# Performance work log

Hardware: AMD Instinct MI355X
Metric: run time of the kernel (lower is better)

Reference implementation:

```python
import jax, jax.numpy as jnp
import numpy as np

N_REL = 8


def setup_inputs() -> dict:
    key = jax.random.key(0)
    ks = jax.random.split(key, 16)
    N, E = 100_000, 1_600_000
    rn = lambda k, shape, s=0.1: jax.random.normal(k, shape, dtype=jnp.float32) * s
    return {
        "x": rn(ks[0], (N, 3), 1.0),
        "edge_index": jax.random.randint(ks[1], (2, E), 0, N),
        "edge_attr": rn(ks[2], (E, 2), 1.0),
        "edge_type": jax.random.randint(ks[3], (E,), 0, N_REL),
        "omega": rn(ks[4], (N, 2), 1.0),
        # encoder weights
        "Wn": rn(ks[5], (3, 64)), "bn": jnp.zeros((64,), jnp.float32),
        "We": rn(ks[6], (2, 32)), "be": jnp.zeros((32,), jnp.float32),
        "Wo": rn(ks[7], (2, 64)), "bo": jnp.zeros((64,), jnp.float32),
        # RGCN layer 1 (edge-feature-aware): per-relation W over concat(x_src, e) -> 64
        "W1": rn(ks[8], (N_REL, 96, 64)), "Wroot1": rn(ks[9], (64, 64)), "b1": jnp.zeros((64,), jnp.float32),
        # RGCN layer 2 (PyG RGCNConv, aggr='max')
        "W2": rn(ks[10], (N_REL, 64, 64)), "Wroot2": rn(ks[11], (64, 64)), "b2": jnp.zeros((64,), jnp.float32),
        # head
        "Wagg": rn(ks[12], (128, 64)), "bagg": jnp.zeros((64,), jnp.float32),
        "Wc": rn(ks[13], (64, 1)), "bc": jnp.zeros((1,), jnp.float32),
    }


def reference(x, edge_index, edge_attr, edge_type, omega,
              Wn, bn, We, be, Wo, bo,
              W1, Wroot1, b1, W2, Wroot2, b2,
              Wagg, bagg, Wc, bc):
    N = x.shape[0]
    n = jax.nn.relu(x @ Wn + bn)            # [N,64]
    e = jax.nn.relu(edge_attr @ We + be)    # [E,32]
    o = jax.nn.relu(omega @ Wo + bo)        # [N,64]
    src, dst = edge_index[0], edge_index[1]

    # --- RGCN layer 1: per-relation transform of [x_src || e], sum-aggregate ---
    feat = jnp.concatenate([n[src], e], axis=1)  # [E,96]
    acc = n @ Wroot1 + b1                        # root/self term
    for r in range(N_REL):
        m = (edge_type == r).astype(feat.dtype)[:, None]
        acc = acc + jax.ops.segment_sum((feat * m) @ W1[r], dst, num_segments=N)
    h = jax.nn.relu(acc)                         # [N,64]

    # --- RGCN layer 2: per-relation transform of x_src, max-aggregate per relation, sum over relations ---
    hs = h[src]                                  # [E,64]
    neg = jnp.finfo(h.dtype).min
    acc2 = h @ Wroot2 + b2
    for r in range(N_REL):
        mask = (edge_type == r)[:, None]
        msg = jnp.where(mask, hs @ W2[r], neg)
        mx = jax.ops.segment_max(msg, dst, num_segments=N)
        acc2 = acc2 + jnp.where(mx > neg * 0.5, mx, 0.0)  # empty segments -> 0 (PyG zeros-init scatter)
    h2 = jax.nn.relu(acc2)                       # [N,64]

    out = jax.nn.relu(jnp.concatenate([h2, o], axis=1) @ Wagg + bagg)
    return jnp.tanh(out @ Wc + bc) * 5.0
```

## Files before the change

kernel.cpp:

```cpp
#include <hip/hip_runtime.h>
#include <cmath>

typedef __attribute__((ext_vector_type(8))) short short8;
typedef __attribute__((ext_vector_type(4))) float floatx4;

__device__ __forceinline__ unsigned short rnbf(float f) {
    unsigned u = __float_as_uint(f);
    u += 0x7fffu + ((u >> 16) & 1u);
    return (unsigned short)(u >> 16);
}
__device__ __forceinline__ float bf2f(unsigned short h) {
    return __uint_as_float(((unsigned)h) << 16);
}
__device__ __forceinline__ int rfl(int v) { return __builtin_amdgcn_readfirstlane(v); }
__device__ __forceinline__ float eAct(unsigned ry, float we0, float we1, float bev) {
    float a0 = __uint_as_float(ry & 0xFFFF0000u);
    float a1 = __uint_as_float(ry << 16);
    return fmaxf(fmaf(a1, we1, fmaf(a0, we0, bev)), 0.f);
}
__device__ __forceinline__ unsigned vidx(int x, unsigned pl, int lane) {
    return (((unsigned)x >> 24) & 7u)*pl + (unsigned)(x & 0xFFFFFF)*64u + (unsigned)lane;
}
__device__ __forceinline__ void mstep(int r, float v, int& cur, float& mx, float& add) {
    bool nb = (r != cur);
    add += nb ? mx : 0.f;
    mx = nb ? v : fmaxf(mx, v);
    cur = r;
}

__global__ void k_histd(const int* __restrict__ ei, const int* __restrict__ et,
                        int* __restrict__ deg8, int E)
{
    int e = blockIdx.x*blockDim.x + threadIdx.x;
    if (e < E) atomicAdd(&deg8[ei[E + e]*8 + et[e]], 1);
}

#define SCHUNK 1024
__global__ void k_bsum(const int* __restrict__ deg, int* __restrict__ bsum, int K)
{
    __shared__ int s[256];
    int b = blockIdx.x, t = threadIdx.x;
    int base = b*SCHUNK;
    int v = 0;
    for (int k = t; k < SCHUNK; k += 256) { int i = base + k; v += (i < K) ? deg[i] : 0; }
    s[t] = v; __syncthreads();
    for (int o = 128; o; o >>= 1) { if (t < o) s[t] += s[t+o]; __syncthreads(); }
    if (t == 0) bsum[b] = s[0];
}
__global__ void k_bscan(int* __restrict__ bsum, int nb)
{
    __shared__ int ts[256];
    int t = threadIdx.x;
    int v[4]; int loc = 0;
    #pragma unroll
    for (int u = 0; u < 4; ++u) { int i = t*4+u; v[u] = (i < nb) ? bsum[i] : 0; loc += v[u]; }
    ts[t] = loc; __syncthreads();
    for (int o = 1; o < 256; o <<= 1) {
        int add = (t >= o) ? ts[t-o] : 0;
        __syncthreads();
        ts[t] += add;
        __syncthreads();
    }
    int excl = ts[t] - loc;
    #pragma unroll
    for (int u = 0; u < 4; ++u) {
        int i = t*4+u;
        if (i < nb) bsum[i] = excl;
        excl += v[u];
    }
}
__global__ void k_bapply(const int* __restrict__ deg, const int* __restrict__ bsum,
                         int* __restrict__ off, int* __restrict__ cursor, int K)
{
    __shared__ int ts[256];
    int b = blockIdx.x, t = threadIdx.x;
    int base = b*SCHUNK;
    int v[4]; int loc = 0;
    #pragma unroll
    for (int u = 0; u < 4; ++u) { int i = base + t*4 + u; v[u] = (i < K) ? deg[i] : 0; loc += v[u]; }
    ts[t] = loc; __syncthreads();
    for (int o = 1; o < 256; o <<= 1) {
        int add = (t >= o) ? ts[t-o] : 0;
        __syncthreads();
        ts[t] += add;
        __syncthreads();
    }
    int excl = ts[t] - loc + bsum[b];
    #pragma unroll
    for (int u = 0; u < 4; ++u) {
        int i = base + t*4 + u;
        if (i < K) { off[i] = excl; cursor[i] = excl; }
        excl += v[u];
        if (i == K-1) off[K] = excl;
    }
}

__global__ void k_scatd(const int* __restrict__ ei, const float* __restrict__ ea,
                        const int* __restrict__ et, int* __restrict__ cursor,
                        int2* __restrict__ srec, int E)
{
    int e = blockIdx.x*blockDim.x + threadIdx.x;
    if (e >= E) return;
    int rel = et[e];
    int key = ei[E + e]*8 + rel;
    int pos = atomicAdd(&cursor[key], 1);
    float2 a = ((const float2*)ea)[e];
    int xv = ei[e] | (rel << 24);
    int yv = ((int)rnbf(a.x) << 16) | (int)rnbf(a.y);
    srec[pos] = make_int2(xv, yv);
}

#define PB_KEYS 4096
#define PA_CH   4096
__global__ void k_binit(const int* __restrict__ off8, int* __restrict__ bktCur,
                        int nbkt, int K8)
{
    int b = blockIdx.x*blockDim.x + threadIdx.x;
    if (b < nbkt) {
        int k = b*PB_KEYS; if (k > K8) k = K8;
        bktCur[b] = off8[k];
    }
}
__global__ __launch_bounds__(256) void k_partA(
    const int* __restrict__ ei, const float* __restrict__ ea,
    const int* __restrict__ et, int* __restrict__ bktCur,
    int2* __restrict__ tmp, int E, int nbkt)
{
    __shared__ int cnt[512], base[512];
    int b0 = blockIdx.x * PA_CH;
    for (int j = threadIdx.x; j < nbkt; j += 256) cnt[j] = 0;
    __syncthreads();
    int2 rec[16]; int bk[16];
    #pragma unroll
    for (int u = 0; u < 16; ++u) {
        int e = b0 + u*256 + threadIdx.x;
        bk[u] = -1;
        if (e < E) {
            int rel = et[e];
            int src = ei[e];
            int dst = ei[E + e];
            float2 a = ((const float2*)ea)[e];
            rec[u] = make_int2(src | (rel << 17) | ((dst & 511) << 20),
                               ((int)rnbf(a.x) << 16) | (int)rnbf(a.y));
            bk[u] = dst >> 9;
            atomicAdd(&cnt[bk[u]], 1);
        }
    }
    __syncthreads();
    for (int j = threadIdx.x; j < nbkt; j += 256) {
        int c = cnt[j];
        base[j] = c ? atomicAdd(&bktCur[j], c) : 0;
    }
    __syncthreads();
    for (int j = threadIdx.x; j < nbkt; j += 256) cnt[j] = 0;
    __syncthreads();
    #pragma unroll
    for (int u = 0; u < 16; ++u) {
        if (bk[u] >= 0) {
            int pos = base[bk[u]] + atomicAdd(&cnt[bk[u]], 1);
            tmp[pos] = rec[u];
        }
    }
}
__global__ __launch_bounds__(256) void k_partB(
    const int2* __restrict__ tmp, const int* __restrict__ off8,
    int2* __restrict__ srec, int K8)
{
    __shared__ int cur[PB_KEYS];
    int kbase = blockIdx.x * PB_KEYS;
    int kend = kbase + PB_KEYS; if (kend > K8) kend = K8;
    int nk = kend - kbase;
    for (int j = threadIdx.x; j < nk; j += 256) cur[j] = off8[kbase + j];
    __syncthreads();
    int bstart = off8[kbase];
    int bend = off8[kend];
    for (int i = bstart + threadIdx.x; i < bend; i += 256) {
        int2 r = tmp[i];
        unsigned xw = (unsigned)r.x;
        int src = (int)(xw & 0x1FFFFu);
        int rel = (int)((xw >> 17) & 7u);
        int dstLow = (int)((xw >> 20) & 511u);
        int pos = atomicAdd(&cur[dstLow*8 + rel], 1);
        srec[pos] = make_int2(src | (rel << 24), r.y);
    }
}

__global__ __launch_bounds__(64) void k_wpack(
    const float* __restrict__ W1, const float* __restrict__ W2,
    const float* __restrict__ Wroot1, const float* __restrict__ Wroot2,
    const float* __restrict__ Wagg, unsigned short* __restrict__ wpk)
{
    int unit = blockIdx.x >> 2;
    int jt = blockIdx.x & 3;
    int lane = threadIdx.x;
    const float* Wb;
    int kbase;
    if (unit < 16) {
        Wb = W1 + (size_t)(unit >> 1)*96*64;
        kbase = (unit & 1)*32;
    } else if (unit < 32) {
        Wb = W2 + (size_t)((unit - 16) >> 1)*64*64;
        kbase = ((unit - 16) & 1)*32;
    } else if (unit < 40) {
        Wb = W1 + (size_t)(unit - 32)*96*64;
        kbase = 64;
    } else if (unit < 42) {
        Wb = Wroot1; kbase = (unit - 40)*32;
    } else if (unit < 44) {
        Wb = Wroot2; kbase = (unit - 42)*32;
    } else {
        Wb = Wagg;   kbase = (unit - 44)*32;
    }
    int j = jt*16 + (lane & 15);
    size_t base = (((size_t)unit*4 + jt)*64 + lane)*16;
    #pragma unroll
    for (int i = 0; i < 8; ++i) {
        int k = kbase + (lane >> 4)*8 + i;
        float f = Wb[(size_t)k*64 + j];
        unsigned short hi = rnbf(f);
        unsigned short lo = rnbf(f - bf2f(hi));
        wpk[base + i] = hi;
        wpk[base + 8 + i] = lo;
    }
}

__global__ __launch_bounds__(256) void k_encB(
    const float* __restrict__ x,
    const float* __restrict__ Wn, const float* __restrict__ bn,
    const unsigned short* __restrict__ wpk, const float* __restrict__ b1,
    float* __restrict__ nbuf, float* __restrict__ acc1, int N)
{
    int lane = threadIdx.x & 63;
    int wave = threadIdx.x >> 6;
    int n0 = blockIdx.x*64 + 16*wave;
    int m = lane & 15, q = lane >> 4;
    #pragma unroll 4
    for (int t = 0; t < 16; ++t) {
        int nd = n0 + t;
        if (nd < N) {
            float x0 = x[3*nd], x1 = x[3*nd+1], x2 = x[3*nd+2];
            float nj = fmaxf(fmaf(x2, Wn[128+lane], fmaf(x1, Wn[64+lane], fmaf(x0, Wn[lane], bn[lane]))), 0.f);
            nbuf[(size_t)nd*64 + lane] = nj;
        }
    }
    int node = n0 + m; if (node >= N) node = N - 1;
    float x0 = x[3*node], x1 = x[3*node+1], x2 = x[3*node+2];
    short8 ah[2], al[2];
    #pragma unroll
    for (int ks = 0; ks < 2; ++ks) {
        #pragma unroll
        for (int i = 0; i < 8; ++i) {
            int f = ks*32 + q*8 + i;
            float nf = fmaxf(fmaf(x2, Wn[128+f], fmaf(x1, Wn[64+f], fmaf(x0, Wn[f], bn[f]))), 0.f);
            unsigned short hb = rnbf(nf);
            ah[ks][i] = (short)hb;
            al[ks][i] = (short)rnbf(nf - bf2f(hb));
        }
    }
    floatx4 acc[4];
    #pragma unroll
    for (int jt = 0; jt < 4; ++jt) acc[jt] = (floatx4){0.f,0.f,0.f,0.f};
    #pragma unroll
    for (int ks = 0; ks < 2; ++ks) {
        int unit = 40 + ks;
        #pragma unroll
        for (int jt = 0; jt < 4; ++jt) {
            const unsigned short* qp = wpk + (((size_t)unit*4 + jt)*64 + lane)*16;
            short8 bh = *(const short8*)qp;
            short8 bl = *(const short8*)(qp + 8);
            acc[jt] = __builtin_amdgcn_mfma_f32_16x16x32_bf16(ah[ks], bh, acc[jt], 0,0,0);
            acc[jt] = __builtin_amdgcn_mfma_f32_16x16x32_bf16(ah[ks], bl, acc[jt], 0,0,0);
            acc[jt] = __builtin_amdgcn_mfma_f32_16x16x32_bf16(al[ks], bh, acc[jt], 0,0,0);
        }
    }
    #pragma unroll
    for (int jt = 0; jt < 4; ++jt) {
        float bb = b1[jt*16 + m];
        #pragma unroll
        for (int t = 0; t < 4; ++t) {
            int row = n0 + q*4 + t;
            if (row < N) acc1[(size_t)row*64 + jt*16 + m] = acc[jt][t] + bb;
        }
    }
}

__global__ __launch_bounds__(256) void k_vgemmB(
    const float* __restrict__ F, const unsigned short* __restrict__ wpk,
    int unitBase, int g0, int Gc, unsigned short* __restrict__ Vbf,
    size_t plane, int N)
{
    int lane = threadIdx.x & 63;
    int wave = threadIdx.x >> 6;
    int n0 = blockIdx.x*64 + 16*wave;
    int m = lane & 15, q = lane >> 4;
    int node = n0 + m;
    if (node >= N) node = N - 1;
    const float4* Fr = (const float4*)(F + (size_t)node*64);
    short8 ah[2], al[2];
    #pragma unroll
    for (int ks = 0; ks < 2; ++ks) {
        float4 u0 = Fr[ks*8 + q*2];
        float4 u1 = Fr[ks*8 + q*2 + 1];
        float fv[8] = {u0.x,u0.y,u0.z,u0.w,u1.x,u1.y,u1.z,u1.w};
        #pragma unroll
        for (int i = 0; i < 8; ++i) {
            unsigned short hb = rnbf(fv[i]);
            ah[ks][i] = (short)hb;
            al[ks][i] = (short)rnbf(fv[i] - bf2f(hb));
        }
    }
    for (int p = 0; p < Gc; ++p) {
        int rel = g0 + p;
        floatx4 acc[4];
        #pragma unroll
        for (int jt = 0; jt < 4; ++jt) acc[jt] = (floatx4){0.f,0.f,0.f,0.f};
        #pragma unroll
        for (int ks = 0; ks < 2; ++ks) {
            int unit = unitBase + rel*2 + ks;
            #pragma unroll
            for (int jt = 0; jt < 4; ++jt) {
                const unsigned short* qp = wpk + (((size_t)unit*4 + jt)*64 + lane)*16;
                short8 bh = *(const short8*)qp;
                short8 bl = *(const short8*)(qp + 8);
                acc[jt] = __builtin_amdgcn_mfma_f32_16x16x32_bf16(ah[ks], bh, acc[jt], 0,0,0);
                acc[jt] = __builtin_amdgcn_mfma_f32_16x16x32_bf16(ah[ks], bl, acc[jt], 0,0,0);
                acc[jt] = __builtin_amdgcn_mfma_f32_16x16x32_bf16(al[ks], bh, acc[jt], 0,0,0);
            }
        }
        unsigned short* Vp = Vbf + (size_t)p*plane;
        #pragma unroll
        for (int jt = 0; jt < 4; ++jt) {
            #pragma unroll
            for (int t = 0; t < 4; ++t) {
                int row = n0 + q*4 + t;
                if (row < N) Vp[(size_t)row*64 + jt*16 + m] = rnbf(acc[jt][t]);
            }
        }
    }
}

__global__ __launch_bounds__(256) void k_agg1ef(
    const int2* __restrict__ srec, const int* __restrict__ off8,
    const unsigned short* __restrict__ Vbf, size_t plane,
    const float* __restrict__ We, const float* __restrict__ be,
    float* __restrict__ acc1, unsigned short* __restrict__ Sep, int N)
{
    int lane = threadIdx.x & 63;
    int wv = threadIdx.x >> 6;
    unsigned pl = (unsigned)plane;
    float we0 = We[lane & 31], we1 = We[32 + (lane & 31)], bev = be[lane & 31];
    int stride = gridDim.x*4;
    for (int node = blockIdx.x*4 + wv; node < N; node += stride) {
        const int* ofp = off8 + node*8;
        int o0 = rfl(ofp[0]), o8 = rfl(ofp[8]);
        float vsum = 0.f;
        int i = o0;
        for (; i + 16 <= o8; i += 16) {
            int2 q[16];
            #pragma unroll
            for (int u = 0; u < 16; ++u) q[u] = srec[i+u];
            int xs[16];
            #pragma unroll
            for (int u = 0; u < 16; ++u) xs[u] = rfl(q[u].x);
            float v[16];
            #pragma unroll
            for (int u = 0; u < 16; ++u) v[u] = bf2f(Vbf[vidx(xs[u], pl, lane)]);
            float s01 = (v[0]+v[1]) + (v[2]+v[3]);
            float s23 = (v[4]+v[5]) + (v[6]+v[7]);
            float s45 = (v[8]+v[9]) + (v[10]+v[11]);
            float s67 = (v[12]+v[13]) + (v[14]+v[15]);
            vsum += (s01 + s23) + (s45 + s67);
        }
        for (; i + 8 <= o8; i += 8) {
            int2 q0 = srec[i+0], q1 = srec[i+1], q2 = srec[i+2], q3 = srec[i+3];
            int2 q4 = srec[i+4], q5 = srec[i+5], q6 = srec[i+6], q7 = srec[i+7];
            int x0 = rfl(q0.x), x1 = rfl(q1.x), x2 = rfl(q2.x), x3 = rfl(q3.x);
            int x4 = rfl(q4.x), x5 = rfl(q5.x), x6 = rfl(q6.x), x7 = rfl(q7.x);
            float v0 = bf2f(Vbf[vidx(x0, pl, lane)]);
            float v1 = bf2f(Vbf[vidx(x1, pl, lane)]);
            float v2 = bf2f(Vbf[vidx(x2, pl, lane)]);
            float v3 = bf2f(Vbf[vidx(x3, pl, lane)]);
            float v4 = bf2f(Vbf[vidx(x4, pl, lane)]);
            float v5 = bf2f(Vbf[vidx(x5, pl, lane)]);
            float v6 = bf2f(Vbf[vidx(x6, pl, lane)]);
            float v7 = bf2f(Vbf[vidx(x7, pl, lane)]);
            vsum += ((v0+v1)+(v2+v3)) + ((v4+v5)+(v6+v7));
        }
        for (; i < o8; ++i) {
            int xx = rfl(srec[i].x);
            vsum += bf2f(Vbf[vidx(xx, pl, lane)]);
        }
        int o1 = rfl(ofp[1]), o2 = rfl(ofp[2]), o3 = rfl(ofp[3]), o4 = rfl(ofp[4]);
        int o5 = rfl(ofp[5]), o6 = rfl(ofp[6]), o7 = rfl(ofp[7]);
        const unsigned* sy = (const unsigned*)srec;
        float se0=0,se1=0,se2=0,se3=0,se4=0,se5=0,se6=0,se7=0;
        #pragma unroll
        for (int r = 0; r < 8; ++r) {
            int s = (r==0)?o0:(r==1)?o1:(r==2)?o2:(r==3)?o3:(r==4)?o4:(r==5)?o5:(r==6)?o6:o7;
            int e = (r==0)?o1:(r==1)?o2:(r==2)?o3:(r==3)?o4:(r==4)?o5:(r==5)?o6:(r==6)?o7:o8;
            if (s == e) continue;
            float ev = 0.f;
            int k = s;
            for (; k + 4 <= e; k += 4) {
                unsigned y0 = sy[2*(k+0)+1], y1 = sy[2*(k+1)+1];
                unsigned y2 = sy[2*(k+2)+1], y3 = sy[2*(k+3)+1];
                ev += eAct(y0, we0, we1, bev);
                ev += eAct(y1, we0, we1, bev);
                ev += eAct(y2, we0, we1, bev);
                ev += eAct(y3, we0, we1, bev);
            }
            for (; k < e; ++k) ev += eAct(sy[2*k+1], we0, we1, bev);
            if (r == 0) se0 = ev;  if (r == 1) se1 = ev;
            if (r == 2) se2 = ev;  if (r == 3) se3 = ev;
            if (r == 4) se4 = ev;  if (r == 5) se5 = ev;
            if (r == 6) se6 = ev;  if (r == 7) se7 = ev;
        }
        unsigned short* Sp = Sep + (size_t)node*256;
        Sp[0*64 + lane] = rnbf((lane < 32) ? se0 : se1);
        Sp[1*64 + lane] = rnbf((lane < 32) ? se2 : se3);
        Sp[2*64 + lane] = rnbf((lane < 32) ? se4 : se5);
        Sp[3*64 + lane] = rnbf((lane < 32) ? se6 : se7);
        if (o0 != o8) acc1[(size_t)node*64 + lane] += vsum;
    }
}

__global__ __launch_bounds__(256) void k_agg1e(
    const int2* __restrict__ srec, const int* __restrict__ off8,
    const unsigned short* __restrict__ Vbf, size_t plane,
    const float* __restrict__ We, const float* __restrict__ be,
    float* __restrict__ acc1, unsigned short* __restrict__ Sep, int N, int Gc)
{
    int lane = threadIdx.x & 63;
    int wv = threadIdx.x >> 6;
    float we0 = We[lane & 31], we1 = We[32 + (lane & 31)], bev = be[lane & 31];
    int stride = gridDim.x*4;
    for (int node = blockIdx.x*4 + wv; node < N; node += stride) {
        int o0 = rfl(off8[node*8+0]), o1 = rfl(off8[node*8+1]), o2 = rfl(off8[node*8+2]);
        int o3 = rfl(off8[node*8+3]), o4 = rfl(off8[node*8+4]), o5 = rfl(off8[node*8+5]);
        int o6 = rfl(off8[node*8+6]), o7 = rfl(off8[node*8+7]), o8 = rfl(off8[node*8+8]);
        float vsum = 0.f;
        float se0=0,se1=0,se2=0,se3=0,se4=0,se5=0,se6=0,se7=0;
        #pragma unroll
        for (int r = 0; r < 8; ++r) {
            int s = (r==0)?o0:(r==1)?o1:(r==2)?o2:(r==3)?o3:(r==4)?o4:(r==5)?o5:(r==6)?o6:o7;
            int e = (r==0)?o1:(r==1)?o2:(r==2)?o3:(r==3)?o4:(r==4)?o5:(r==5)?o6:(r==6)?o7:o8;
            if (s == e) continue;
            const unsigned short* Vp = Vbf + (size_t)r*plane;
            bool doV = (r < Gc);
            float ev = 0.f;
            int i = s;
            for (; i + 8 <= e; i += 8) {
                int2 q0 = srec[i+0], q1 = srec[i+1], q2 = srec[i+2], q3 = srec[i+3];
                int2 q4 = srec[i+4], q5 = srec[i+5], q6 = srec[i+6], q7 = srec[i+7];
                if (doV) {
                    float v0 = bf2f(Vp[(size_t)(rfl(q0.x) & 0xFFFFFF)*64 + lane]);
                    float v1 = bf2f(Vp[(size_t)(rfl(q1.x) & 0xFFFFFF)*64 + lane]);
                    float v2 = bf2f(Vp[(size_t)(rfl(q2.x) & 0xFFFFFF)*64 + lane]);
                    float v3 = bf2f(Vp[(size_t)(rfl(q3.x) & 0xFFFFFF)*64 + lane]);
                    float v4 = bf2f(Vp[(size_t)(rfl(q4.x) & 0xFFFFFF)*64 + lane]);
                    float v5 = bf2f(Vp[(size_t)(rfl(q5.x) & 0xFFFFFF)*64 + lane]);
                    float v6 = bf2f(Vp[(size_t)(rfl(q6.x) & 0xFFFFFF)*64 + lane]);
                    float v7 = bf2f(Vp[(size_t)(rfl(q7.x) & 0xFFFFFF)*64 + lane]);
                    vsum += ((v0+v1)+(v2+v3)) + ((v4+v5)+(v6+v7));
                }
                ev += eAct((unsigned)q0.y, we0, we1, bev);
                ev += eAct((unsigned)q1.y, we0, we1, bev);
                ev += eAct((unsigned)q2.y, we0, we1, bev);
                ev += eAct((unsigned)q3.y, we0, we1, bev);
                ev += eAct((unsigned)q4.y, we0, we1, bev);
                ev += eAct((unsigned)q5.y, we0, we1, bev);
                ev += eAct((unsigned)q6.y, we0, we1, bev);
                ev += eAct((unsigned)q7.y, we0, we1, bev);
            }
            for (; i < e; ++i) {
                int2 qq = srec[i];
                if (doV) vsum += bf2f(Vp[(size_t)(rfl(qq.x) & 0xFFFFFF)*64 + lane]);
                ev += eAct((unsigned)qq.y, we0, we1, bev);
            }
            if (r == 0) se0 = ev;  if (r == 1) se1 = ev;
            if (r == 2) se2 = ev;  if (r == 3) se3 = ev;
            if (r == 4) se4 = ev;  if (r == 5) se5 = ev;
            if (r == 6) se6 = ev;  if (r == 7) se7 = ev;
        }
        unsigned short* Sp = Sep + (size_t)node*256;
        Sp[0*64 + lane] = rnbf((lane < 32) ? se0 : se1);
        Sp[1*64 + lane] = rnbf((lane < 32) ? se2 : se3);
        Sp[2*64 + lane] = rnbf((lane < 32) ? se4 : se5);
        Sp[3*64 + lane] = rnbf((lane < 32) ? se6 : se7);
        if (o0 != o8) acc1[(size_t)node*64 + lane] += vsum;
    }
}

__global__ __launch_bounds__(256) void k_agg1v(
    const int2* __restrict__ srec, const int* __restrict__ off8,
    const unsigned short* __restrict__ Vbf, size_t plane,
    float* __restrict__ acc1, int N, int g0, int g1)
{
    int lane = threadIdx.x & 63;
    int wv = threadIdx.x >> 6;
    int stride = gridDim.x*4;
    for (int node = blockIdx.x*4 + wv; node < N; node += stride) {
        float vsum = 0.f;
        bool any = false;
        for (int r = g0; r < g1; ++r) {
            int s = rfl(off8[node*8 + r]);
            int e = rfl(off8[node*8 + r + 1]);
            if (s == e) continue;
            any = true;
            const unsigned short* Vp = Vbf + (size_t)(r - g0)*plane;
            int i = s;
            for (; i + 8 <= e; i += 8) {
                int s0 = rfl(srec[i+0].x) & 0xFFFFFF, s1 = rfl(srec[i+1].x) & 0xFFFFFF;
                int s2 = rfl(srec[i+2].x) & 0xFFFFFF, s3 = rfl(srec[i+3].x) & 0xFFFFFF;
                int s4 = rfl(srec[i+4].x) & 0xFFFFFF, s5 = rfl(srec[i+5].x) & 0xFFFFFF;
                int s6 = rfl(srec[i+6].x) & 0xFFFFFF, s7 = rfl(srec[i+7].x) & 0xFFFFFF;
                float v0 = bf2f(Vp[(size_t)s0*64 + lane]), v1 = bf2f(Vp[(size_t)s1*64 + lane]);
                float v2 = bf2f(Vp[(size_t)s2*64 + lane]), v3 = bf2f(Vp[(size_t)s3*64 + lane]);
                float v4 = bf2f(Vp[(size_t)s4*64 + lane]), v5 = bf2f(Vp[(size_t)s5*64 + lane]);
                float v6 = bf2f(Vp[(size_t)s6*64 + lane]), v7 = bf2f(Vp[(size_t)s7*64 + lane]);
                vsum += ((v0+v1)+(v2+v3)) + ((v4+v5)+(v6+v7));
            }
            for (; i < e; ++i) {
                int sx = rfl(srec[i].x) & 0xFFFFFF;
                vsum += bf2f(Vp[(size_t)sx*64 + lane]);
            }
        }
        if (any) acc1[(size_t)node*64 + lane] += vsum;
    }
}

__global__ __launch_bounds__(256) void k_segemm(
    const unsigned short* __restrict__ Sep, const unsigned short* __restrict__ wpk,
    float* __restrict__ acc1, int N)
{
    int lane = threadIdx.x & 63;
    int wave = threadIdx.x >> 6;
    int n0 = blockIdx.x*64 + 16*wave;
    int m = lane & 15, q = lane >> 4;
    int node = n0 + m;
    if (node >= N) node = N - 1;
    floatx4 acc[4];
    #pragma unroll
    for (int jt = 0; jt < 4; ++jt) acc[jt] = (floatx4){0.f,0.f,0.f,0.f};
    for (int rel = 0; rel < 8; ++rel) {
        short8 ah = *(const short8*)(Sep + (size_t)node*256 + rel*32 + q*8);
        int unit = 32 + rel;
        #pragma unroll
        for (int jt = 0; jt < 4; ++jt) {
            const unsigned short* qp = wpk + (((size_t)unit*4 + jt)*64 + lane)*16;
            short8 bh = *(const short8*)qp;
            short8 bl = *(const short8*)(qp + 8);
            acc[jt] = __builtin_amdgcn_mfma_f32_16x16x32_bf16(ah, bh, acc[jt], 0,0,0);
            acc[jt] = __builtin_amdgcn_mfma_f32_16x16x32_bf16(ah, bl, acc[jt], 0,0,0);
        }
    }
    #pragma unroll
    for (int jt = 0; jt < 4; ++jt) {
        #pragma unroll
        for (int t = 0; t < 4; ++t) {
            int row = n0 + q*4 + t;
            if (row < N) acc1[(size_t)row*64 + jt*16 + m] += acc[jt][t];
        }
    }
}

__global__ __launch_bounds__(256) void k_hrowB(
    float* __restrict__ acc1, float* __restrict__ acc2,
    const unsigned short* __restrict__ wpk, const float* __restrict__ b2, int N)
{
    int lane = threadIdx.x & 63;
    int wave = threadIdx.x >> 6;
    int n0 = blockIdx.x*64 + 16*wave;
    int m = lane & 15, q = lane >> 4;
    int node = n0 + m;
    if (node >= N) node = N - 1;
    float4* Fr = (float4*)(acc1 + (size_t)node*64);
    short8 ah[2], al[2];
    #pragma unroll
    for (int ks = 0; ks < 2; ++ks) {
        float4 u0 = Fr[ks*8 + q*2];
        float4 u1 = Fr[ks*8 + q*2 + 1];
        float fv[8] = {u0.x,u0.y,u0.z,u0.w,u1.x,u1.y,u1.z,u1.w};
        #pragma unroll
        for (int i = 0; i < 8; ++i) {
            float hv = fmaxf(fv[i], 0.f);
            fv[i] = hv;
            unsigned short hb = rnbf(hv);
            ah[ks][i] = (short)hb;
            al[ks][i] = (short)rnbf(hv - bf2f(hb));
        }
        Fr[ks*8 + q*2]     = make_float4(fv[0], fv[1], fv[2], fv[3]);
        Fr[ks*8 + q*2 + 1] = make_float4(fv[4], fv[5], fv[6], fv[7]);
    }
    floatx4 acc[4];
    #pragma unroll
    for (int jt = 0; jt < 4; ++jt) acc[jt] = (floatx4){0.f,0.f,0.f,0.f};
    #pragma unroll
    for (int ks = 0; ks < 2; ++ks) {
        int unit = 42 + ks;
        #pragma unroll
        for (int jt = 0; jt < 4; ++jt) {
            const unsigned short* qp = wpk + (((size_t)unit*4 + jt)*64 + lane)*16;
            short8 bh = *(const short8*)qp;
            short8 bl = *(const short8*)(qp + 8);
            acc[jt] = __builtin_amdgcn_mfma_f32_16x16x32_bf16(ah[ks], bh, acc[jt], 0,0,0);
            acc[jt] = __builtin_amdgcn_mfma_f32_16x16x32_bf16(ah[ks], bl, acc[jt], 0,0,0);
            acc[jt] = __builtin_amdgcn_mfma_f32_16x16x32_bf16(al[ks], bh, acc[jt], 0,0,0);
        }
    }
    #pragma unroll
    for (int jt = 0; jt < 4; ++jt) {
        float bb = b2[jt*16 + m];
        #pragma unroll
        for (int t = 0; t < 4; ++t) {
            int row = n0 + q*4 + t;
            if (row < N) acc2[(size_t)row*64 + jt*16 + m] = acc[jt][t] + bb;
        }
    }
}

__global__ __launch_bounds__(256) void k_agg2f(
    const int2* __restrict__ srec, const int* __restrict__ off8,
    const unsigned short* __restrict__ Ubf, size_t plane,
    float* __restrict__ acc2, int N)
{
    int lane = threadIdx.x & 63;
    int wv = threadIdx.x >> 6;
    unsigned pl = (unsigned)plane;
    int stride = gridDim.x*4;
    for (int node = blockIdx.x*4 + wv; node < N; node += stride) {
        int o0 = rfl(off8[node*8]);
        int o8 = rfl(off8[node*8 + 8]);
        if (o0 == o8) continue;
        float add = 0.f, mx = 0.f;
        int cur = -1;
        int i = o0;
        for (; i + 16 <= o8; i += 16) {
            int2 q[16];
            #pragma unroll
            for (int u = 0; u < 16; ++u) q[u] = srec[i+u];
            int xs[16];
            #pragma unroll
            for (int u = 0; u < 16; ++u) xs[u] = rfl(q[u].x);
            float v[16];
            #pragma unroll
            for (int u = 0; u < 16; ++u) v[u] = bf2f(Ubf[vidx(xs[u], pl, lane)]);
            #pragma unroll
            for (int u = 0; u < 16; ++u)
                mstep((int)(((unsigned)xs[u] >> 24) & 7u), v[u], cur, mx, add);
        }
        for (; i + 8 <= o8; i += 8) {
            int2 q0 = srec[i+0], q1 = srec[i+1], q2 = srec[i+2], q3 = srec[i+3];
            int2 q4 = srec[i+4], q5 = srec[i+5], q6 = srec[i+6], q7 = srec[i+7];
            int x0 = rfl(q0.x), x1 = rfl(q1.x), x2 = rfl(q2.x), x3 = rfl(q3.x);
            int x4 = rfl(q4.x), x5 = rfl(q5.x), x6 = rfl(q6.x), x7 = rfl(q7.x);
            float v0 = bf2f(Ubf[vidx(x0, pl, lane)]);
            float v1 = bf2f(Ubf[vidx(x1, pl, lane)]);
            float v2 = bf2f(Ubf[vidx(x2, pl, lane)]);
            float v3 = bf2f(Ubf[vidx(x3, pl, lane)]);
            float v4 = bf2f(Ubf[vidx(x4, pl, lane)]);
            float v5 = bf2f(Ubf[vidx(x5, pl, lane)]);
            float v6 = bf2f(Ubf[vidx(x6, pl, lane)]);
            float v7 = bf2f(Ubf[vidx(x7, pl, lane)]);
            mstep((int)(((unsigned)x0 >> 24) & 7u), v0, cur, mx, add);
            mstep((int)(((unsigned)x1 >> 24) & 7u), v1, cur, mx, add);
            mstep((int)(((unsigned)x2 >> 24) & 7u), v2, cur, mx, add);
            mstep((int)(((unsigned)x3 >> 24) & 7u), v3, cur, mx, add);
            mstep((int)(((unsigned)x4 >> 24) & 7u), v4, cur, mx, add);
            mstep((int)(((unsigned)x5 >> 24) & 7u), v5, cur, mx, add);
            mstep((int)(((unsigned)x6 >> 24) & 7u), v6, cur, mx, add);
            mstep((int)(((unsigned)x7 >> 24) & 7u), v7, cur, mx, add);
        }
        for (; i < o8; ++i) {
            int xx = rfl(srec[i].x);
            float v = bf2f(Ubf[vidx(xx, pl, lane)]);
            mstep((int)(((unsigned)xx >> 24) & 7u), v, cur, mx, add);
        }
        add += mx;
        acc2[(size_t)node*64 + lane] += add;
    }
}

__global__ __launch_bounds__(256) void k_agg2(
    const int2* __restrict__ srec, const int* __restrict__ off8,
    const unsigned short* __restrict__ Ubf, size_t plane,
    float* __restrict__ acc2, int N, int g0, int g1)
{
    int lane = threadIdx.x & 63;
    int wv = threadIdx.x >> 6;
    int stride = gridDim.x*4;
    const float NEG = -__builtin_inff();
    for (int node = blockIdx.x*4 + wv; node < N; node += stride) {
        float add = 0.f;
        bool any = false;
        for (int r = g0; r < g1; ++r) {
            int s = rfl(off8[node*8 + r]);
            int e = rfl(off8[node*8 + r + 1]);
            if (s == e) continue;
            any = true;
            const unsigned short* Up = Ubf + (size_t)(r - g0)*plane;
            float mx = NEG;
            int i = s;
            for (; i + 8 <= e; i += 8) {
                int s0 = rfl(srec[i+0].x) & 0xFFFFFF, s1 = rfl(srec[i+1].x) & 0xFFFFFF;
                int s2 = rfl(srec[i+2].x) & 0xFFFFFF, s3 = rfl(srec[i+3].x) & 0xFFFFFF;
                int s4 = rfl(srec[i+4].x) & 0xFFFFFF, s5 = rfl(srec[i+5].x) & 0xFFFFFF;
                int s6 = rfl(srec[i+6].x) & 0xFFFFFF, s7 = rfl(srec[i+7].x) & 0xFFFFFF;
                float v0 = bf2f(Up[(size_t)s0*64 + lane]), v1 = bf2f(Up[(size_t)s1*64 + lane]);
                float v2 = bf2f(Up[(size_t)s2*64 + lane]), v3 = bf2f(Up[(size_t)s3*64 + lane]);
                float v4 = bf2f(Up[(size_t)s4*64 + lane]), v5 = bf2f(Up[(size_t)s5*64 + lane]);
                float v6 = bf2f(Up[(size_t)s6*64 + lane]), v7 = bf2f(Up[(size_t)s7*64 + lane]);
                float m01 = fmaxf(v0, v1), m23 = fmaxf(v2, v3);
                float m45 = fmaxf(v4, v5), m67 = fmaxf(v6, v7);
                mx = fmaxf(mx, fmaxf(fmaxf(m01, m23), fmaxf(m45, m67)));
            }
            for (; i < e; ++i) {
                int sx = rfl(srec[i].x) & 0xFFFFFF;
                mx = fmaxf(mx, bf2f(Up[(size_t)sx*64 + lane]));
            }
            add += mx;
        }
        if (any) acc2[(size_t)node*64 + lane] += add;
    }
}

__global__ __launch_bounds__(256) void k_finB(
    const float* __restrict__ acc2, const float* __restrict__ omega,
    const float* __restrict__ Wo, const float* __restrict__ bo,
    const unsigned short* __restrict__ wpk,
    const float* __restrict__ bagg, const float* __restrict__ Wc,
    const float* __restrict__ bc, float* __restrict__ out, int N)
{
    int lane = threadIdx.x & 63;
    int wave = threadIdx.x >> 6;
    int n0 = blockIdx.x*64 + 16*wave;
    int m = lane & 15, q = lane >> 4;
    int node = n0 + m;
    if (node >= N) node = N - 1;
    short8 ah[4], al[4];
    const float4* Fr = (const float4*)(acc2 + (size_t)node*64);
    #pragma unroll
    for (int ks = 0; ks < 2; ++ks) {
        float4 u0 = Fr[ks*8 + q*2];
        float4 u1 = Fr[ks*8 + q*2 + 1];
        float fv[8] = {u0.x,u0.y,u0.z,u0.w,u1.x,u1.y,u1.z,u1.w};
        #pragma unroll
        for (int i = 0; i < 8; ++i) {
            float hv = fmaxf(fv[i], 0.f);
            unsigned short hb = rnbf(hv);
            ah[ks][i] = (short)hb;
            al[ks][i] = (short)rnbf(hv - bf2f(hb));
        }
    }
    float om0 = omega[2*node], om1 = omega[2*node+1];
    #pragma unroll
    for (int ks = 2; ks < 4; ++ks) {
        #pragma unroll
        for (int i = 0; i < 8; ++i) {
            int f = (ks - 2)*32 + q*8 + i;
            float ov = fmaxf(fmaf(om1, Wo[64+f], fmaf(om0, Wo[f], bo[f])), 0.f);
            unsigned short hb = rnbf(ov);
            ah[ks][i] = (short)hb;
            al[ks][i] = (short)rnbf(ov - bf2f(hb));
        }
    }
    floatx4 acc[4];
    #pragma unroll
    for (int jt = 0; jt < 4; ++jt) acc[jt] = (floatx4){0.f,0.f,0.f,0.f};
    #pragma unroll
    for (int ks = 0; ks < 4; ++ks) {
        int unit = 44 + ks;
        #pragma unroll
        for (int jt = 0; jt < 4; ++jt) {
            const unsigned short* qp = wpk + (((size_t)unit*4 + jt)*64 + lane)*16;
            short8 bh = *(const short8*)qp;
            short8 bl = *(const short8*)(qp + 8);
            acc[jt] = __builtin_amdgcn_mfma_f32_16x16x32_bf16(ah[ks], bh, acc[jt], 0,0,0);
            acc[jt] = __builtin_amdgcn_mfma_f32_16x16x32_bf16(ah[ks], bl, acc[jt], 0,0,0);
            acc[jt] = __builtin_amdgcn_mfma_f32_16x16x32_bf16(al[ks], bh, acc[jt], 0,0,0);
        }
    }
    float bg0 = bagg[m], bg1 = bagg[16+m], bg2 = bagg[32+m], bg3 = bagg[48+m];
    float wc0 = Wc[m],   wc1 = Wc[16+m],   wc2 = Wc[32+m],   wc3 = Wc[48+m];
    float bc0 = bc[0];
    #pragma unroll
    for (int t = 0; t < 4; ++t) {
        float s = fmaxf(acc[0][t] + bg0, 0.f)*wc0
                + fmaxf(acc[1][t] + bg1, 0.f)*wc1
                + fmaxf(acc[2][t] + bg2, 0.f)*wc2
                + fmaxf(acc[3][t] + bg3, 0.f)*wc3;
        s += __shfl_xor(s, 1);
        s += __shfl_xor(s, 2);
        s += __shfl_xor(s, 4);
        s += __shfl_xor(s, 8);
        int row = n0 + q*4 + t;
        if (m == 0 && row < N) out[row] = tanhf(s + bc0) * 5.0f;
    }
}

extern "C" void kernel_launch(void* const* d_in, const int* in_sizes, int n_in,
                              void* d_out, int out_size, void* d_ws, size_t ws_size,
                              hipStream_t stream)
{
    const float* x      = (const float*)d_in[0];
    const int*   ei     = (const int*)d_in[1];
    const float* ea     = (const float*)d_in[2];
    const int*   et     = (const int*)d_in[3];
    const float* omega  = (const float*)d_in[4];
    const float* Wn     = (const float*)d_in[5];
    const float* bn     = (const float*)d_in[6];
    const float* We     = (const float*)d_in[7];
    const float* be     = (const float*)d_in[8];
    const float* Wo     = (const float*)d_in[9];
    const float* bo     = (const float*)d_in[10];
    const float* W1     = (const float*)d_in[11];
    const float* Wroot1 = (const float*)d_in[12];
    const float* b1     = (const float*)d_in[13];
    const float* W2     = (const float*)d_in[14];
    const float* Wroot2 = (const float*)d_in[15];
    const float* b2     = (const float*)d_in[16];
    const float* Wagg   = (const float*)d_in[17];
    const float* bagg   = (const float*)d_in[18];
    const float* Wc     = (const float*)d_in[19];
    const float* bc     = (const float*)d_in[20];
    int N = in_sizes[0] / 3;
    int E = in_sizes[3];
    float* out = (float*)d_out;

    int K8 = N*8;
    int nb = (K8 + SCHUNK - 1)/SCHUNK;

    #define ALIGN256(p) ((char*)(((size_t)(p) + 255) & ~(size_t)255))
    char* pp = (char*)d_ws;
    float* nbuf   = (float*)pp;  pp = ALIGN256(pp + (size_t)N*64*4);
    float* acc1   = (float*)pp;  pp = ALIGN256(pp + (size_t)N*64*4);
    int2*  srec   = (int2*)pp;   pp = ALIGN256(pp + (size_t)E*8);
    int*   deg8   = (int*)pp;    pp = ALIGN256(pp + (size_t)K8*4);
    int*   off8   = (int*)pp;    pp = ALIGN256(pp + (size_t)(K8+1)*4);
    int*   cursor = (int*)pp;    pp = ALIGN256(pp + (size_t)K8*4);
    int*   bsum   = (int*)pp;    pp = ALIGN256(pp + (size_t)nb*4);
    int*   bktCur = (int*)pp;    pp = ALIGN256(pp + (size_t)512*4);
    unsigned short* wpk = (unsigned short*)pp;
    pp = ALIGN256(pp + (size_t)48*4*64*16*2);
    unsigned short* Sepool = (unsigned short*)pp;
    pp = ALIGN256(pp + (size_t)N*256*2);
    size_t off = (size_t)(pp - (char*)d_ws);
    size_t planeElems = (size_t)N*64;
    size_t avail = (ws_size > off) ? (ws_size - off) : 0;
    int G = (int)(avail / (planeElems*2));
    if (G > 8) G = 8;
    if (G < 1) G = 1;
    unsigned short* Vbf = (unsigned short*)pp;
    float* acc2 = nbuf;

    int gblocks = (N + 63)/64;
    k_wpack<<<192, 64, 0, stream>>>(W1, W2, Wroot1, Wroot2, Wagg, wpk);
    k_encB<<<gblocks, 256, 0, stream>>>(x, Wn, bn, wpk, b1, nbuf, acc1, N);
    hipMemsetAsync(deg8, 0, (size_t)K8*4, stream);
    k_histd<<<(E + 255)/256, 256, 0, stream>>>(ei, et, deg8, E);
    k_bsum<<<nb, 256, 0, stream>>>(deg8, bsum, K8);
    k_bscan<<<1, 256, 0, stream>>>(bsum, nb);
    k_bapply<<<nb, 256, 0, stream>>>(deg8, bsum, off8, cursor, K8);

    int nbkt = (N + 511) >> 9;
    bool fastSort = (N <= 131072) && ((size_t)E*8 <= (size_t)N*256*2);
    if (fastSort) {
        int2* tmp = (int2*)Sepool;
        k_binit<<<(nbkt + 255)/256, 256, 0, stream>>>(off8, bktCur, nbkt, K8);
        k_partA<<<(E + PA_CH - 1)/PA_CH, 256, 0, stream>>>(ei, ea, et, bktCur, tmp, E, nbkt);
        k_partB<<<nbkt, 256, 0, stream>>>(tmp, off8, srec, K8);
    } else {
        k_scatd<<<(E + 255)/256, 256, 0, stream>>>(ei, ea, et, cursor, srec, E);
    }

    int aggBlocks = 4096;
    if (G == 8) {
        k_vgemmB<<<gblocks, 256, 0, stream>>>(nbuf, wpk, 0, 0, 8, Vbf, planeElems, N);
        k_agg1ef<<<aggBlocks, 256, 0, stream>>>(srec, off8, Vbf, planeElems, We, be,
                                                acc1, Sepool, N);
    } else {
        int Gc1 = G;
        k_vgemmB<<<gblocks, 256, 0, stream>>>(nbuf, wpk, 0, 0, Gc1, Vbf, planeElems, N);
        k_agg1e<<<aggBlocks, 256, 0, stream>>>(srec, off8, Vbf, planeElems, We, be,
                                               acc1, Sepool, N, Gc1);
        for (int g0 = Gc1; g0 < 8; g0 += G) {
            int Gc = (8 - g0 < G) ? (8 - g0) : G;
            k_vgemmB<<<gblocks, 256, 0, stream>>>(nbuf, wpk, 0, g0, Gc, Vbf, planeElems, N);
            k_agg1v<<<aggBlocks, 256, 0, stream>>>(srec, off8, Vbf, planeElems,
                                                   acc1, N, g0, g0 + Gc);
        }
    }
    k_segemm<<<gblocks, 256, 0, stream>>>(Sepool, wpk, acc1, N);
    k_hrowB<<<gblocks, 256, 0, stream>>>(acc1, acc2, wpk, b2, N);
    if (G == 8) {
        k_vgemmB<<<gblocks, 256, 0, stream>>>(acc1, wpk, 16, 0, 8, Vbf, planeElems, N);
        k_agg2f<<<aggBlocks, 256, 0, stream>>>(srec, off8, Vbf, planeElems, acc2, N);
    } else {
        for (int g0 = 0; g0 < 8; g0 += G) {
            int Gc = (8 - g0 < G) ? (8 - g0) : G;
            k_vgemmB<<<gblocks, 256, 0, stream>>>(acc1, wpk, 16, g0, Gc, Vbf, planeElems, N);
            k_agg2<<<aggBlocks, 256, 0, stream>>>(srec, off8, Vbf, planeElems,
                                                  acc2, N, g0, g0 + Gc);
        }
    }
    k_finB<<<gblocks, 256, 0, stream>>>(acc2, omega, Wo, bo, wpk, bagg, Wc, bc, out, N);
}
```

Before: 546.1 us.

## Fuse encoder/root/V-gemm kernels and replace full key histogram with bucket-level sort

Fuses the node encoder, layer-1 root GEMM and per-relation V projection into one kernel (k_encV), and fuses the edge-feature segment GEMM, ReLU, layer-2 root GEMM and layer-2 V projection into another (k_seghrowV). This removes the intermediate nbuf round-trip and several launches. The fast sort path drops the full per-(dst,rel) histogram and three-kernel scan. It uses a coarse 512-node bucket count instead, and each partB2 block computes its own fine offsets in shared memory. The cost is recomputing the encoder activations inside each fused kernel and extra shared-memory scan work per bucket.

```diff
diff --git a/kernel.cpp b/kernel.cpp
--- a/kernel.cpp
+++ b/kernel.cpp
@@ -34,7 +34,6 @@
     int e = blockIdx.x*blockDim.x + threadIdx.x;
     if (e < E) atomicAdd(&deg8[ei[E + e]*8 + et[e]], 1);
 }
-
 #define SCHUNK 1024
 __global__ void k_bsum(const int* __restrict__ deg, int* __restrict__ bsum, int K)
 {
@@ -94,7 +93,6 @@
         if (i == K-1) off[K] = excl;
     }
 }
-
 __global__ void k_scatd(const int* __restrict__ ei, const float* __restrict__ ea,
                         const int* __restrict__ et, int* __restrict__ cursor,
                         int2* __restrict__ srec, int E)
@@ -112,14 +110,37 @@
 
 #define PB_KEYS 4096
 #define PA_CH   4096
-__global__ void k_binit(const int* __restrict__ off8, int* __restrict__ bktCur,
-                        int nbkt, int K8)
-{
-    int b = blockIdx.x*blockDim.x + threadIdx.x;
-    if (b < nbkt) {
-        int k = b*PB_KEYS; if (k > K8) k = K8;
-        bktCur[b] = off8[k];
-    }
+__global__ __launch_bounds__(256) void k_cnt256(
+    const int* __restrict__ ei, int* __restrict__ bktCnt, int E, int nbkt)
+{
+    __shared__ int cnt[512];
+    for (int j = threadIdx.x; j < nbkt; j += 256) cnt[j] = 0;
+    __syncthreads();
+    int stride = gridDim.x*256;
+    for (int e = blockIdx.x*256 + threadIdx.x; e < E; e += stride)
+        atomicAdd(&cnt[ei[E + e] >> 9], 1);
+    __syncthreads();
+    for (int j = threadIdx.x; j < nbkt; j += 256) {
+        int c = cnt[j];
+        if (c) atomicAdd(&bktCnt[j], c);
+    }
+}
+__global__ void k_scan256(const int* __restrict__ bktCnt, int* __restrict__ bktBase,
+                          int* __restrict__ bktCur, int nbkt)
+{
+    __shared__ int ts[256];
+    int t = threadIdx.x;
+    int v = (t < nbkt) ? bktCnt[t] : 0;
+    ts[t] = v; __syncthreads();
+    for (int o = 1; o < 256; o <<= 1) {
+        int add = (t >= o) ? ts[t-o] : 0;
+        __syncthreads();
+        ts[t] += add;
+        __syncthreads();
+    }
+    int excl = ts[t] - v;
+    if (t < nbkt) { bktBase[t] = excl; bktCur[t] = excl; }
+    if (t == nbkt - 1) bktBase[nbkt] = excl + v;
 }
 __global__ __launch_bounds__(256) void k_partA(
     const int* __restrict__ ei, const float* __restrict__ ea,
@@ -162,25 +183,54 @@
         }
     }
 }
-__global__ __launch_bounds__(256) void k_partB(
-    const int2* __restrict__ tmp, const int* __restrict__ off8,
-    int2* __restrict__ srec, int K8)
-{
-    __shared__ int cur[PB_KEYS];
-    int kbase = blockIdx.x * PB_KEYS;
+__global__ __launch_bounds__(256) void k_partB2(
+    const int2* __restrict__ tmp, const int* __restrict__ bktBase,
+    int* __restrict__ off8, int2* __restrict__ srec, int K8)
+{
+    __shared__ int cnt[PB_KEYS];
+    __shared__ int ts[256];
+    int b = blockIdx.x;
+    int kbase = b * PB_KEYS;
     int kend = kbase + PB_KEYS; if (kend > K8) kend = K8;
     int nk = kend - kbase;
-    for (int j = threadIdx.x; j < nk; j += 256) cur[j] = off8[kbase + j];
+    int bstart = bktBase[b];
+    int bend = bktBase[b + 1];
+    int t = threadIdx.x;
+    for (int j = t; j < PB_KEYS; j += 256) cnt[j] = 0;
     __syncthreads();
-    int bstart = off8[kbase];
-    int bend = off8[kend];
-    for (int i = bstart + threadIdx.x; i < bend; i += 256) {
+    for (int i = bstart + t; i < bend; i += 256) {
+        unsigned xw = (unsigned)tmp[i].x;
+        int key = (int)((xw >> 20) & 511u)*8 + (int)((xw >> 17) & 7u);
+        atomicAdd(&cnt[key], 1);
+    }
+    __syncthreads();
+    int loc[16]; int lsum = 0;
+    #pragma unroll
+    for (int u = 0; u < 16; ++u) { loc[u] = cnt[t*16 + u]; lsum += loc[u]; }
+    ts[t] = lsum; __syncthreads();
+    for (int o = 1; o < 256; o <<= 1) {
+        int add = (t >= o) ? ts[t-o] : 0;
+        __syncthreads();
+        ts[t] += add;
+        __syncthreads();
+    }
+    int excl = ts[t] - lsum + bstart;
+    #pragma unroll
+    for (int u = 0; u < 16; ++u) {
+        int j = t*16 + u;
+        cnt[j] = excl;
+        if (j < nk) off8[kbase + j] = excl;
+        excl += loc[u];
+    }
+    if (t == 0 && kend == K8) off8[K8] = bend;
+    __syncthreads();
+    for (int i = bstart + t; i < bend; i += 256) {
         int2 r = tmp[i];
         unsigned xw = (unsigned)r.x;
         int src = (int)(xw & 0x1FFFFu);
         int rel = (int)((xw >> 17) & 7u);
-        int dstLow = (int)((xw >> 20) & 511u);
-        int pos = atomicAdd(&cur[dstLow*8 + rel], 1);
+        int key = (int)((xw >> 20) & 511u)*8 + rel;
+        int pos = atomicAdd(&cnt[key], 1);
         srec[pos] = make_int2(src | (rel << 24), r.y);
     }
 }
@@ -221,6 +271,87 @@
         unsigned short lo = rnbf(f - bf2f(hi));
         wpk[base + i] = hi;
         wpk[base + 8 + i] = lo;
+    }
+}
+
+__global__ __launch_bounds__(256) void k_encV(
+    const float* __restrict__ x,
+    const float* __restrict__ Wn, const float* __restrict__ bn,
+    const unsigned short* __restrict__ wpk, const float* __restrict__ b1,
+    float* __restrict__ acc1, unsigned short* __restrict__ Vbf,
+    size_t plane, int N)
+{
+    int lane = threadIdx.x & 63;
+    int wave = threadIdx.x >> 6;
+    int n0 = blockIdx.x*64 + 16*wave;
+    int m = lane & 15, q = lane >> 4;
+    int node = n0 + m; if (node >= N) node = N - 1;
+    float x0 = x[3*node], x1 = x[3*node+1], x2 = x[3*node+2];
+    short8 ah[2], al[2];
+    #pragma unroll
+    for (int ks = 0; ks < 2; ++ks) {
+        #pragma unroll
+        for (int i = 0; i < 8; ++i) {
+            int f = ks*32 + q*8 + i;
+            float nf = fmaxf(fmaf(x2, Wn[128+f], fmaf(x1, Wn[64+f], fmaf(x0, Wn[f], bn[f]))), 0.f);
+            unsigned short hb = rnbf(nf);
+            ah[ks][i] = (short)hb;
+            al[ks][i] = (short)rnbf(nf - bf2f(hb));
+        }
+    }
+    {
+        floatx4 acc[4];
+        #pragma unroll
+        for (int jt = 0; jt < 4; ++jt) acc[jt] = (floatx4){0.f,0.f,0.f,0.f};
+        #pragma unroll
+        for (int ks = 0; ks < 2; ++ks) {
+            int unit = 40 + ks;
+            #pragma unroll
+            for (int jt = 0; jt < 4; ++jt) {
+                const unsigned short* qp = wpk + (((size_t)unit*4 + jt)*64 + lane)*16;
+                short8 bh = *(const short8*)qp;
+                short8 bl = *(const short8*)(qp + 8);
+                acc[jt] = __builtin_amdgcn_mfma_f32_16x16x32_bf16(ah[ks], bh, acc[jt], 0,0,0);
+                acc[jt] = __builtin_amdgcn_mfma_f32_16x16x32_bf16(ah[ks], bl, acc[jt], 0,0,0);
+                acc[jt] = __builtin_amdgcn_mfma_f32_16x16x32_bf16(al[ks], bh, acc[jt], 0,0,0);
+            }
+        }
+        #pragma unroll
+        for (int jt = 0; jt < 4; ++jt) {
+            float bb = b1[jt*16 + m];
+            #pragma unroll
+            for (int t = 0; t < 4; ++t) {
+                int row = n0 + q*4 + t;
+                if (row < N) acc1[(size_t)row*64 + jt*16 + m] = acc[jt][t] + bb;
+            }
+        }
+    }
+    for (int p = 0; p < 8; ++p) {
+        floatx4 acc[4];
+        #pragma unroll
+        for (int jt = 0; jt < 4; ++jt) acc[jt] = (floatx4){0.f,0.f,0.f,0.f};
+        #pragma unroll
+        for (int ks = 0; ks < 2; ++ks) {
+            int unit = p*2 + ks;
+            #pragma unroll
+            for (int jt = 0; jt < 4; ++jt) {
+                const unsigned short* qp = wpk + (((size_t)unit*4 + jt)*64 + lane)*16;
+                short8 bh = *(const short8*)qp;
+                short8 bl = *(const short8*)(qp + 8);
+                acc[jt] = __builtin_amdgcn_mfma_f32_16x16x32_bf16(ah[ks], bh, acc[jt], 0,0,0);
+                acc[jt] = __builtin_amdgcn_mfma_f32_16x16x32_bf16(ah[ks], bl, acc[jt], 0,0,0);
+                acc[jt] = __builtin_amdgcn_mfma_f32_16x16x32_bf16(al[ks], bh, acc[jt], 0,0,0);
+            }
+        }
+        unsigned short* Vp = Vbf + (size_t)p*plane;
+        #pragma unroll
+        for (int jt = 0; jt < 4; ++jt) {
+            #pragma unroll
+            for (int t = 0; t < 4; ++t) {
+                int row = n0 + q*4 + t;
+                if (row < N) Vp[(size_t)row*64 + jt*16 + m] = rnbf(acc[jt][t]);
+            }
+        }
     }
 }
 
@@ -619,6 +750,114 @@
     }
 }
 
+__global__ __launch_bounds__(256) void k_seghrowV(
+    const unsigned short* __restrict__ Sep, const unsigned short* __restrict__ wpk,
+    const float* __restrict__ acc1, float* __restrict__ acc2,
+    const float* __restrict__ b2, unsigned short* __restrict__ Vbf,
+    size_t plane, int N)
+{
+    __shared__ __align__(16) float sS[4][16][68];
+    int lane = threadIdx.x & 63;
+    int wave = threadIdx.x >> 6;
+    int n0 = blockIdx.x*64 + 16*wave;
+    int m = lane & 15, q = lane >> 4;
+    int node = n0 + m;
+    if (node >= N) node = N - 1;
+    {
+        floatx4 sacc[4];
+        #pragma unroll
+        for (int jt = 0; jt < 4; ++jt) sacc[jt] = (floatx4){0.f,0.f,0.f,0.f};
+        for (int rel = 0; rel < 8; ++rel) {
+            short8 sa = *(const short8*)(Sep + (size_t)node*256 + rel*32 + q*8);
+            int unit = 32 + rel;
+            #pragma unroll
+            for (int jt = 0; jt < 4; ++jt) {
+                const unsigned short* qp = wpk + (((size_t)unit*4 + jt)*64 + lane)*16;
+                short8 bh = *(const short8*)qp;
+                short8 bl = *(const short8*)(qp + 8);
+                sacc[jt] = __builtin_amdgcn_mfma_f32_16x16x32_bf16(sa, bh, sacc[jt], 0,0,0);
+                sacc[jt] = __builtin_amdgcn_mfma_f32_16x16x32_bf16(sa, bl, sacc[jt], 0,0,0);
+            }
+        }
+        #pragma unroll
+        for (int jt = 0; jt < 4; ++jt) {
+            #pragma unroll
+            for (int t = 0; t < 4; ++t)
+                sS[wave][q*4 + t][jt*16 + m] = sacc[jt][t];
+        }
+    }
+    __syncthreads();
+    const float4* Fr = (const float4*)(acc1 + (size_t)node*64);
+    short8 ah[2], al[2];
+    #pragma unroll
+    for (int ks = 0; ks < 2; ++ks) {
+        float4 u0 = Fr[ks*8 + q*2];
+        float4 u1 = Fr[ks*8 + q*2 + 1];
+        float fv[8] = {u0.x,u0.y,u0.z,u0.w,u1.x,u1.y,u1.z,u1.w};
+        #pragma unroll
+        for (int i = 0; i < 8; ++i) {
+            float hv = fmaxf(fv[i] + sS[wave][m][ks*32 + q*8 + i], 0.f);
+            unsigned short hb = rnbf(hv);
+            ah[ks][i] = (short)hb;
+            al[ks][i] = (short)rnbf(hv - bf2f(hb));
+        }
+    }
+    {
+        floatx4 acc[4];
+        #pragma unroll
+        for (int jt = 0; jt < 4; ++jt) acc[jt] = (floatx4){0.f,0.f,0.f,0.f};
+        #pragma unroll
+        for (int ks = 0; ks < 2; ++ks) {
+            int unit = 42 + ks;
+            #pragma unroll
+            for (int jt = 0; jt < 4; ++jt) {
+                const unsigned short* qp = wpk + (((size_t)unit*4 + jt)*64 + lane)*16;
+                short8 bh = *(const short8*)qp;
+                short8 bl = *(const short8*)(qp + 8);
+                acc[jt] = __builtin_amdgcn_mfma_f32_16x16x32_bf16(ah[ks], bh, acc[jt], 0,0,0);
+                acc[jt] = __builtin_amdgcn_mfma_f32_16x16x32_bf16(ah[ks], bl, acc[jt], 0,0,0);
+                acc[jt] = __builtin_amdgcn_mfma_f32_16x16x32_bf16(al[ks], bh, acc[jt], 0,0,0);
+            }
+        }
+        #pragma unroll
+        for (int jt = 0; jt < 4; ++jt) {
+            float bb = b2[jt*16 + m];
+            #pragma unroll
+            for (int t = 0; t < 4; ++t) {
+                int row = n0 + q*4 + t;
+                if (row < N) acc2[(size_t)row*64 + jt*16 + m] = acc[jt][t] + bb;
+            }
+        }
+    }
+    for (int p = 0; p < 8; ++p) {
+        floatx4 acc[4];
+        #pragma unroll
+        for (int jt = 0; jt < 4; ++jt) acc[jt] = (floatx4){0.f,0.f,0.f,0.f};
+        #pragma unroll
+        for (int ks = 0; ks < 2; ++ks) {
+            int unit = 16 + p*2 + ks;
+            #pragma unroll
+            for (int jt = 0; jt < 4; ++jt) {
+                const unsigned short* qp = wpk + (((size_t)unit*4 + jt)*64 + lane)*16;
+                short8 bh = *(const short8*)qp;
+                short8 bl = *(const short8*)(qp + 8);
+                acc[jt] = __builtin_amdgcn_mfma_f32_16x16x32_bf16(ah[ks], bh, acc[jt], 0,0,0);
+                acc[jt] = __builtin_amdgcn_mfma_f32_16x16x32_bf16(ah[ks], bl, acc[jt], 0,0,0);
+                acc[jt] = __builtin_amdgcn_mfma_f32_16x16x32_bf16(al[ks], bh, acc[jt], 0,0,0);
+            }
+        }
+        unsigned short* Vp = Vbf + (size_t)p*plane;
+        #pragma unroll
+        for (int jt = 0; jt < 4; ++jt) {
+            #pragma unroll
+            for (int t = 0; t < 4; ++t) {
+                int row = n0 + q*4 + t;
+                if (row < N) Vp[(size_t)row*64 + jt*16 + m] = rnbf(acc[jt][t]);
+            }
+        }
+    }
+}
+
 __global__ __launch_bounds__(256) void k_agg2f(
     const int2* __restrict__ srec, const int* __restrict__ off8,
     const unsigned short* __restrict__ Ubf, size_t plane,
@@ -840,6 +1079,7 @@
     int*   cursor = (int*)pp;    pp = ALIGN256(pp + (size_t)K8*4);
     int*   bsum   = (int*)pp;    pp = ALIGN256(pp + (size_t)nb*4);
     int*   bktCur = (int*)pp;    pp = ALIGN256(pp + (size_t)512*4);
+    int*   bktBase= (int*)pp;    pp = ALIGN256(pp + (size_t)520*4);
     unsigned short* wpk = (unsigned short*)pp;
     pp = ALIGN256(pp + (size_t)48*4*64*16*2);
     unsigned short* Sepool = (unsigned short*)pp;
@@ -854,30 +1094,39 @@
     float* acc2 = nbuf;
 
     int gblocks = (N + 63)/64;
-    k_wpack<<<192, 64, 0, stream>>>(W1, W2, Wroot1, Wroot2, Wagg, wpk);
-    k_encB<<<gblocks, 256, 0, stream>>>(x, Wn, bn, wpk, b1, nbuf, acc1, N);
-    hipMemsetAsync(deg8, 0, (size_t)K8*4, stream);
-    k_histd<<<(E + 255)/256, 256, 0, stream>>>(ei, et, deg8, E);
-    k_bsum<<<nb, 256, 0, stream>>>(deg8, bsum, K8);
-    k_bscan<<<1, 256, 0, stream>>>(bsum, nb);
-    k_bapply<<<nb, 256, 0, stream>>>(deg8, bsum, off8, cursor, K8);
-
     int nbkt = (N + 511) >> 9;
     bool fastSort = (N <= 131072) && ((size_t)E*8 <= (size_t)N*256*2);
+
+    k_wpack<<<192, 64, 0, stream>>>(W1, W2, Wroot1, Wroot2, Wagg, wpk);
+    if (G == 8) {
+        k_encV<<<gblocks, 256, 0, stream>>>(x, Wn, bn, wpk, b1, acc1, Vbf, planeElems, N);
+    } else {
+        k_encB<<<gblocks, 256, 0, stream>>>(x, Wn, bn, wpk, b1, nbuf, acc1, N);
+    }
+
     if (fastSort) {
         int2* tmp = (int2*)Sepool;
-        k_binit<<<(nbkt + 255)/256, 256, 0, stream>>>(off8, bktCur, nbkt, K8);
+        hipMemsetAsync(deg8, 0, (size_t)nbkt*4, stream);
+        k_cnt256<<<1024, 256, 0, stream>>>(ei, deg8, E, nbkt);
+        k_scan256<<<1, 256, 0, stream>>>(deg8, bktBase, bktCur, nbkt);
         k_partA<<<(E + PA_CH - 1)/PA_CH, 256, 0, stream>>>(ei, ea, et, bktCur, tmp, E, nbkt);
-        k_partB<<<nbkt, 256, 0, stream>>>(tmp, off8, srec, K8);
+        k_partB2<<<nbkt, 256, 0, stream>>>(tmp, bktBase, off8, srec, K8);
     } else {
+        hipMemsetAsync(deg8, 0, (size_t)K8*4, stream);
+        k_histd<<<(E + 255)/256, 256, 0, stream>>>(ei, et, deg8, E);
+        k_bsum<<<nb, 256, 0, stream>>>(deg8, bsum, K8);
+        k_bscan<<<1, 256, 0, stream>>>(bsum, nb);
+        k_bapply<<<nb, 256, 0, stream>>>(deg8, bsum, off8, cursor, K8);
         k_scatd<<<(E + 255)/256, 256, 0, stream>>>(ei, ea, et, cursor, srec, E);
     }
 
     int aggBlocks = 4096;
     if (G == 8) {
-        k_vgemmB<<<gblocks, 256, 0, stream>>>(nbuf, wpk, 0, 0, 8, Vbf, planeElems, N);
         k_agg1ef<<<aggBlocks, 256, 0, stream>>>(srec, off8, Vbf, planeElems, We, be,
                                                 acc1, Sepool, N);
+        k_seghrowV<<<gblocks, 256, 0, stream>>>(Sepool, wpk, acc1, acc2, b2,
+                                                Vbf, planeElems, N);
+        k_agg2f<<<aggBlocks, 256, 0, stream>>>(srec, off8, Vbf, planeElems, acc2, N);
     } else {
         int Gc1 = G;
         k_vgemmB<<<gblocks, 256, 0, stream>>>(nbuf, wpk, 0, 0, Gc1, Vbf, planeElems, N);
@@ -889,13 +1138,8 @@
             k_agg1v<<<aggBlocks, 256, 0, stream>>>(srec, off8, Vbf, planeElems,
                                                    acc1, N, g0, g0 + Gc);
         }
-    }
-    k_segemm<<<gblocks, 256, 0, stream>>>(Sepool, wpk, acc1, N);
-    k_hrowB<<<gblocks, 256, 0, stream>>>(acc1, acc2, wpk, b2, N);
-    if (G == 8) {
-        k_vgemmB<<<gblocks, 256, 0, stream>>>(acc1, wpk, 16, 0, 8, Vbf, planeElems, N);
-        k_agg2f<<<aggBlocks, 256, 0, stream>>>(srec, off8, Vbf, planeElems, acc2, N);
-    } else {
+        k_segemm<<<gblocks, 256, 0, stream>>>(Sepool, wpk, acc1, N);
+        k_hrowB<<<gblocks, 256, 0, stream>>>(acc1, acc2, wpk, b2, N);
         for (int g0 = 0; g0 < 8; g0 += G) {
             int Gc = (8 - g0 < G) ? (8 - g0) : G;
             k_vgemmB<<<gblocks, 256, 0, stream>>>(acc1, wpk, 16, g0, Gc, Vbf, planeElems, N);
```

Result: faster. 469.4 us (-14.1%).
